# Kernel tuning notes

Measured on AMD Instinct MI355X. Metric: run time of the kernel, lower is better.

Reference implementation:

```python
import jax, jax.numpy as jnp
import numpy as np
import math

# dims: batch, in-channels, freq bins, frames(=cropsize), ffn dim, bands
B, C, BINS, W, FF, NB = 16, 8, 1024, 256, 2048, 4
EPS = 1e-5


def _ln(x, g, b):
    m = x.mean(-1, keepdims=True)
    v = ((x - m) ** 2).mean(-1, keepdims=True)
    return (x - m) / jnp.sqrt(v + EPS) * g + b


def _conv1d(x, w, groups=1):
    # x: [b, Cin, L], w: [Cout, Cin//groups, K], 'same' padding
    pad = (w.shape[-1] - 1) // 2
    return jax.lax.conv_general_dilated(
        x, w, (1,), [(pad, pad)],
        dimension_numbers=('NCH', 'OIH', 'NCH'), feature_group_count=groups)


def _mb_attn(x, mem, qw, qb, kw, kb, vw, vb, ow, ob, er, dist_w):
    # MultibandFrameAttention with skewed relative-position bias
    b, w, c = x.shape
    d = c // NB
    q = (x @ qw.T + qb).reshape(b, w, NB, d).transpose(0, 2, 1, 3)    # [b,nb,w,d]
    k = (mem @ kw.T + kb).reshape(b, w, NB, d).transpose(0, 2, 3, 1)  # [b,nb,d,w]
    v = (mem @ vw.T + vb).reshape(b, w, NB, d).transpose(0, 2, 1, 3)  # [b,nb,w,d]
    # skew trick: q @ er -> pad left on last dim -> transpose -> drop first row
    qer = jnp.einsum('bnwd,dc->bnwc', q, er)                           # [b,nb,w,W]
    skew = jnp.pad(qer, ((0, 0), (0, 0), (0, 0), (1, 0)))
    skew = skew.transpose(0, 1, 3, 2)[:, :, 1:, :]                     # [b,nb,W,w]
    idx = jnp.arange(w)
    dist = jnp.abs(idx[:, None] - idx[None, :]).astype(x.dtype) / 2.0  # [w,w]
    p = dist[None] * dist_w + skew                                     # [b,nb,w,w]
    qk = jnp.einsum('bnwd,bndk->bnwk', q, k) / math.sqrt(c)
    a = jax.nn.softmax(qk + p, axis=-1)
    o = jnp.einsum('bnwk,bnkd->bnwd', a, v).transpose(0, 2, 1, 3).reshape(b, w, c)
    return o @ ow.T + ob


def setup_inputs() -> dict:
    key = jax.random.key(0)
    ks = jax.random.split(key, 24)
    rn = lambda k, s, sc=0.02: jax.random.normal(k, s, dtype=jnp.float32) * sc
    d = BINS // NB
    ones = lambda n: jnp.ones((n,), jnp.float32)
    zeros = lambda n: jnp.zeros((n,), jnp.float32)
    return {
        'x': jax.random.normal(ks[0], (B, C, BINS, W), jnp.float32),
        'bott_w': rn(ks[1], (1, C), 0.3),
        'bn_g': ones(1), 'bn_b': zeros(1), 'bn_m': zeros(1), 'bn_v': ones(1),
        'glu_w': rn(ks[2], (2 * BINS, BINS)),
        'n1g': ones(BINS), 'n1b': zeros(BINS),
        'c1L_w': rn(ks[3], (2 * FF, BINS)),
        'c1R_w': rn(ks[4], (FF // 2, BINS, 3)),
        'n2g': ones(2 * FF), 'n2b': zeros(2 * FF),
        'c2dw_w': rn(ks[5], (2 * FF, 1, 9), 0.1),
        'c2pw_w': rn(ks[6], (FF // 2, 2 * FF)),
        'n3g': ones(BINS), 'n3b': zeros(BINS),
        'qw': rn(ks[7], (BINS, BINS)), 'qb': zeros(BINS),
        'kw': rn(ks[8], (BINS, BINS)), 'kb': zeros(BINS),
        'vw': rn(ks[9], (BINS, BINS)), 'vb': zeros(BINS),
        'ow': rn(ks[10], (BINS, BINS)), 'ob': zeros(BINS),
        'er': rn(ks[11], (d, W), 0.02),
        'dist_w': rn(ks[12], (NB, W, 1), 0.02),
        'n4g': ones(BINS), 'n4b': zeros(BINS),
        'c3_w': rn(ks[13], (2 * FF, BINS)),
        'c4_w': rn(ks[14], (BINS, 2 * FF)),
        'n5g': ones(BINS), 'n5b': zeros(BINS),
    }


def reference(x, bott_w, bn_g, bn_b, bn_m, bn_v, glu_w, n1g, n1b,
              c1L_w, c1R_w, n2g, n2b, c2dw_w, c2pw_w, n3g, n3b,
              qw, qb, kw, kb, vw, vb, ow, ob, er, dist_w,
              n4g, n4b, c3_w, c4_w, n5g, n5b):
    # bottleneck: Linear(C->1) over channel dim, BatchNorm2d(1) eval, ReLU
    h0 = jnp.einsum('bchw,oc->bohw', x, bott_w)                        # [b,1,bins,w]
    h0 = (h0 - bn_m[None, :, None, None]) / jnp.sqrt(bn_v[None, :, None, None] + EPS)
    h0 = jax.nn.relu(h0 * bn_g[None, :, None, None] + bn_b[None, :, None, None])
    xs = h0[:, 0].transpose(0, 2, 1)                                   # [b,w,bins]

    # GLU block
    g = xs @ glu_w.T
    a, bgate = g[..., :BINS], g[..., BINS:]
    xs = _ln(xs + a * jax.nn.sigmoid(bgate), n1g, n1b)

    # conv/linear FFN
    hL = jax.nn.relu(xs @ c1L_w.T)                                     # [b,w,2ff]
    hR = jax.nn.relu(_conv1d(xs.transpose(0, 2, 1), c1R_w).transpose(0, 2, 1))
    hR = jnp.pad(hR, ((0, 0), (0, 0), (0, hL.shape[2] - hR.shape[2])))
    h = _ln(hL + hR, n2g, n2b)
    t = _conv1d(h.transpose(0, 2, 1), c2dw_w, groups=2 * FF)           # depthwise
    t = jnp.einsum('bcl,oc->bol', t, c2pw_w).transpose(0, 2, 1)        # [b,w,ff//2]
    t = jnp.pad(t, ((0, 0), (0, 0), (0, xs.shape[2] - t.shape[2])))
    xs = _ln(xs + t, n3g, n3b)

    # multiband attention (self)
    h = _mb_attn(xs, xs, qw, qb, kw, kb, vw, vb, ow, ob, er, dist_w)
    xs = _ln(xs + h, n4g, n4b)

    # final FFN
    h = jax.nn.relu(xs @ c3_w.T) @ c4_w.T
    xs = _ln(xs + h, n5g, n5b)
    return xs.transpose(0, 2, 1)[:, None]                              # [b,1,bins,w]
```

## Files before the change

### kernel.cpp

```cpp
#include <hip/hip_runtime.h>
#include <hip/hip_bf16.h>

#define EPSF 1e-5f

typedef unsigned short u16;
typedef unsigned int   u32;
typedef __attribute__((ext_vector_type(8))) short bf16x8;
typedef __attribute__((ext_vector_type(4))) float f32x4;

#define SWZ(row) (((row) & 7) << 3)

__device__ __forceinline__ u16 f2bf(float f) {
    u32 u = __builtin_bit_cast(u32, f);
    u32 r = u + 0x7fffu + ((u >> 16) & 1u);
    return (u16)(r >> 16);
}
__device__ __forceinline__ float bf2f(u16 h) {
    return __builtin_bit_cast(float, (u32)h << 16);
}
__device__ __forceinline__ float4 bf4f(ushort4 v) {
    return make_float4(bf2f(v.x), bf2f(v.y), bf2f(v.z), bf2f(v.w));
}
__device__ __forceinline__ ushort4 f4bf(float a, float b, float c, float d) {
    ushort4 o; o.x = f2bf(a); o.y = f2bf(b); o.z = f2bf(c); o.w = f2bf(d); return o;
}
__device__ __forceinline__ void gld16(void* lds, const void* gsrc) {
    __builtin_amdgcn_global_load_lds(
        (const __attribute__((address_space(1))) u32*)gsrc,
        (__attribute__((address_space(3))) u32*)lds, 16, 0, 0);
}

__device__ __forceinline__ float wred_sum(float v) {
#pragma unroll
    for (int off = 32; off; off >>= 1) v += __shfl_xor(v, off, 64);
    return v;
}
__device__ __forceinline__ void block_red2(float& s1, float& s2, int tid) {
    __shared__ float red[8];
    s1 = wred_sum(s1); s2 = wred_sum(s2);
    const int lane = tid & 63, wid = tid >> 6;
    if (!lane) { red[wid] = s1; red[4 + wid] = s2; }
    __syncthreads();
    s1 = red[0] + red[1] + red[2] + red[3];
    s2 = red[4] + red[5] + red[6] + red[7];
}

struct SetupArgs {
    const float* ws[9]; u16* wd[9]; int wn[9];
    const float* c1r; u16* c1rd;
    const float* er;  u16* erd;
    const float* dw;  float* dwd;
    const float* qb;  const float* kb; const float* vb; float* bcat;
    u16* zp;
    int off[15];
};
__global__ __launch_bounds__(256)
void setup_k(SetupArgs a)
{
    const int b = blockIdx.x;
    int seg = 0;
    while (seg < 13 && b >= a.off[seg + 1]) ++seg;
    const int i = (b - a.off[seg]) * 256 + threadIdx.x;
    if (seg < 9) {
        if (i < a.wn[seg]) {
            const float4 v = ((const float4*)a.ws[seg])[i];
            const float s = (seg == 6) ? 0.03125f : 1.f;
            ((ushort4*)a.wd[seg])[i] = f4bf(v.x * s, v.y * s, v.z * s, v.w * s);
        }
    } else if (seg == 9) {
        if (i < 3145728) {
            const int q = i / 3072, rem = i - q * 3072;
            const int ks = rem >> 10, ci = rem & 1023;
            a.c1rd[i] = f2bf(a.c1r[((long)q * 1024 + ci) * 3 + ks]);
        }
    } else if (seg == 10) {
        if (i < 65536) { const int c = i >> 8, d = i & 255; a.erd[i] = f2bf(a.er[d * 256 + c]); }
    } else if (seg == 11) {
        if (i < 36864) { const int k = i >> 12, c = i & 4095; a.dwd[i] = a.dw[c * 9 + k]; }
    } else if (seg == 12) {
        if (i < 3072) {
            const float* s = (i < 1024) ? a.qb : ((i < 2048) ? a.kb : a.vb);
            float v = s[i & 1023];
            if (i >= 1024 && i < 2048) v *= 0.03125f;
            a.bcat[i] = v;
        }
    } else {
        if (i < 8192) a.zp[i] = 0;
    }
}

__global__ __launch_bounds__(256)
void bottleneck_k(const float* __restrict__ x, const float* __restrict__ bw,
                  const float* __restrict__ bn_g, const float* __restrict__ bn_b,
                  const float* __restrict__ bn_m, const float* __restrict__ bn_v,
                  u16* __restrict__ xsb)
{
    __shared__ float tile[32][33];
    const int b = blockIdx.z, h0 = blockIdx.y * 32, w0 = blockIdx.x * 32;
    const int tid = threadIdx.x, c = tid & 31, r = tid >> 5;
    float wreg[8];
#pragma unroll
    for (int ch = 0; ch < 8; ++ch) wreg[ch] = bw[ch];
    const float sc = bn_g[0] * rsqrtf(bn_v[0] + EPSF);
    const float sh = bn_b[0] - bn_m[0] * sc;
#pragma unroll
    for (int it = 0; it < 4; ++it) {
        const int h = h0 + r + it * 8;
        const int w = w0 + c;
        float acc = 0.f;
#pragma unroll
        for (int ch = 0; ch < 8; ++ch)
            acc += x[(((long)b * 8 + ch) * 1024 + h) * 256 + w] * wreg[ch];
        tile[r + it * 8][c] = fmaxf(acc * sc + sh, 0.f);
    }
    __syncthreads();
#pragma unroll
    for (int it = 0; it < 4; ++it) {
        const int wl = r + it * 8;
        xsb[((long)b * 256 + w0 + wl) * 1024 + h0 + c] = f2bf(tile[c][wl]);
    }
}

template<int ACT, int OUTBF, int BIAS, int SPLITK>
__global__ __launch_bounds__(512, 2)
void gemm8_k(const u16* __restrict__ A, const u16* __restrict__ B,
             const float* __restrict__ bias, void* __restrict__ Cout,
             int N, int K , int lda, int ldb, long partStride)
{
    extern __shared__ u16 lds[];
    const int m0 = blockIdx.y * 256, n0 = blockIdx.x * 256;
    const int koff = (SPLITK > 1) ? blockIdx.z * K : 0;
    const int nt = K >> 6;
    const int tid = threadIdx.x;
    const int lane = tid & 63, wid = tid >> 6;
    const int wr = ((wid >> 2) & 1) * 128;
    const int wc = (wid & 3) * 64;
    const int l15 = lane & 15, l4 = lane >> 4;

    const u16* Ag = A + (long)m0 * lda + koff;
    const u16* Bg = B + (long)n0 * ldb + koff;

    auto stage = [&](const u16* g, int ld, int ldsbase, int kcol, int h) {
#pragma unroll
        for (int is = 0; is < 2; ++is) {
            const int r = h * 128 + is * 64 + (tid >> 3);
            const int sc = ((tid & 7) * 8) ^ SWZ(r);
            gld16(&lds[ldsbase + h * 8192 + is * 4096 + tid * 8],
                  g + (long)r * ld + kcol + sc);
        }
    };
    auto frag = [&](int base, int row, int col) -> bf16x8 {
        return *(const bf16x8*)&lds[base + row * 64 + (col ^ SWZ(row))];
    };

    f32x4 acc[8][4] = {};

    stage(Ag, lda, 0, 0, 0);
    stage(Ag, lda, 0, 0, 1);
    stage(Bg, ldb, 32768, 0, 0);
    stage(Bg, ldb, 32768, 0, 1);
    if (nt > 1) {
        stage(Bg, ldb, 49152, 64, 0);
        stage(Bg, ldb, 49152, 64, 1);
        stage(Ag, lda, 16384, 64, 0);
        asm volatile("s_waitcnt vmcnt(6)" ::: "memory");
    } else {
        asm volatile("s_waitcnt vmcnt(0)" ::: "memory");
    }
    __builtin_amdgcn_s_barrier();

    for (int kt = 0; kt < nt; ++kt) {
        const int cs = kt & 1;
        const int ab = cs * 16384;
        const int bb = 32768 + cs * 16384;
        const int abn = (cs ^ 1) * 16384;
        const int kc1 = (kt + 1) * 64, kc2 = (kt + 2) * 64;
        bf16x8 alo[4][2], ahi[4][2], b01[2][2], b23[2][2];

#pragma unroll
        for (int i = 0; i < 4; ++i)
#pragma unroll
            for (int kk = 0; kk < 2; ++kk)
                alo[i][kk] = frag(ab, wr + i * 16 + l15, kk * 32 + l4 * 8);
#pragma unroll
        for (int j = 0; j < 2; ++j)
#pragma unroll
            for (int kk = 0; kk < 2; ++kk)
                b01[j][kk] = frag(bb, wc + j * 16 + l15, kk * 32 + l4 * 8);
        if (kt + 1 < nt) stage(Ag, lda, abn, kc1, 1);
        __builtin_amdgcn_s_barrier();
        asm volatile("s_waitcnt lgkmcnt(0)" ::: "memory");
        __builtin_amdgcn_s_setprio(1);
#pragma unroll
        for (int i = 0; i < 4; ++i)
#pragma unroll
            for (int j = 0; j < 2; ++j)
#pragma unroll
                for (int kk = 0; kk < 2; ++kk)
                    acc[i][j] = __builtin_amdgcn_mfma_f32_16x16x32_bf16(alo[i][kk], b01[j][kk], acc[i][j], 0, 0, 0);
        __builtin_amdgcn_s_setprio(0);
        __builtin_amdgcn_s_barrier();

#pragma unroll
        for (int j = 0; j < 2; ++j)
#pragma unroll
            for (int kk = 0; kk < 2; ++kk)
                b23[j][kk] = frag(bb, wc + (j + 2) * 16 + l15, kk * 32 + l4 * 8);
        if (kt + 2 < nt) stage(Bg, ldb, bb, kc2, 0);
        __builtin_amdgcn_s_barrier();
        asm volatile("s_waitcnt lgkmcnt(0)" ::: "memory");
        __builtin_amdgcn_s_setprio(1);
#pragma unroll
        for (int i = 0; i < 4; ++i)
#pragma unroll
            for (int j = 0; j < 2; ++j)
#pragma unroll
                for (int kk = 0; kk < 2; ++kk)
                    acc[i][j + 2] = __builtin_amdgcn_mfma_f32_16x16x32_bf16(alo[i][kk], b23[j][kk], acc[i][j + 2], 0, 0, 0);
        __builtin_amdgcn_s_setprio(0);
        __builtin_amdgcn_s_barrier();

#pragma unroll
        for (int i = 0; i < 4; ++i)
#pragma unroll
            for (int kk = 0; kk < 2; ++kk)
                ahi[i][kk] = frag(ab, wr + (i + 4) * 16 + l15, kk * 32 + l4 * 8);
        if (kt + 2 < nt) stage(Bg, ldb, bb, kc2, 1);
        __builtin_amdgcn_s_barrier();
        asm volatile("s_waitcnt lgkmcnt(0)" ::: "memory");
        __builtin_amdgcn_s_setprio(1);
#pragma unroll
        for (int i = 0; i < 4; ++i)
#pragma unroll
            for (int j = 0; j < 2; ++j)
#pragma unroll
                for (int kk = 0; kk < 2; ++kk)
                    acc[i + 4][j + 2] = __builtin_amdgcn_mfma_f32_16x16x32_bf16(ahi[i][kk], b23[j][kk], acc[i + 4][j + 2], 0, 0, 0);
        __builtin_amdgcn_s_setprio(0);
        __builtin_amdgcn_s_barrier();

        if (kt + 2 < nt) stage(Ag, lda, ab, kc2, 0);
        __builtin_amdgcn_s_barrier();
        __builtin_amdgcn_s_setprio(1);
#pragma unroll
        for (int i = 0; i < 4; ++i)
#pragma unroll
            for (int j = 0; j < 2; ++j)
#pragma unroll
                for (int kk = 0; kk < 2; ++kk)
                    acc[i + 4][j] = __builtin_amdgcn_mfma_f32_16x16x32_bf16(ahi[i][kk], b01[j][kk], acc[i + 4][j], 0, 0, 0);
        __builtin_amdgcn_s_setprio(0);
        if (kt + 2 < nt) {
            asm volatile("s_waitcnt vmcnt(6)" ::: "memory");
        } else {
            asm volatile("s_waitcnt vmcnt(0)" ::: "memory");
        }
        __builtin_amdgcn_s_barrier();
    }

    if (SPLITK > 1) {
        u16* Cp = (u16*)Cout + (long)blockIdx.z * partStride;
#pragma unroll
        for (int i = 0; i < 8; ++i)
#pragma unroll
            for (int j = 0; j < 4; ++j) {
                const int n = n0 + wc + j * 16 + l15;
#pragma unroll
                for (int q = 0; q < 4; ++q) {
                    const int m = m0 + wr + i * 16 + l4 * 4 + q;
                    Cp[(long)m * N + n] = f2bf(acc[i][j][q]);
                }
            }
    } else {
        float* Cf = (float*)Cout;
        u16*   Cb = (u16*)Cout;
#pragma unroll
        for (int i = 0; i < 8; ++i)
#pragma unroll
            for (int j = 0; j < 4; ++j) {
                const int n = n0 + wc + j * 16 + l15;
                const float bv = BIAS ? bias[n] : 0.f;
#pragma unroll
                for (int q = 0; q < 4; ++q) {
                    const int m = m0 + wr + i * 16 + l4 * 4 + q;
                    float v = acc[i][j][q] + bv;
                    if (ACT) v = fmaxf(v, 0.f);
                    if (OUTBF) Cb[(long)m * N + n] = f2bf(v);
                    else       Cf[(long)m * N + n] = v;
                }
            }
    }
}

__global__ __launch_bounds__(512, 2)
void ffconv8_k(const u16* __restrict__ Xb, const u16* __restrict__ Wl,
               const u16* __restrict__ Wr, const u16* __restrict__ zp,
               u16* __restrict__ Hout, u16* __restrict__ Cp3)
{
    extern __shared__ u16 lds[];
    const int bx = blockIdx.x;
    const int m0 = blockIdx.y * 256;
    const bool conv = bx >= 16;
    const int tap  = conv ? ((bx - 16) >> 2) : 0;
    const int shift = conv ? (tap - 1) : 0;
    const int n0 = conv ? (((bx - 16) & 3) * 256) : (bx * 256);
    const u16* Bbase = conv ? (Wr + (long)n0 * 3072 + tap * 1024)
                            : (Wl + (long)n0 * 1024);
    const int ldb = conv ? 3072 : 1024;
    const int nt = 16;
    const int tid = threadIdx.x;
    const int lane = tid & 63, wid = tid >> 6;
    const int wr = ((wid >> 2) & 1) * 128;
    const int wc = (wid & 3) * 64;
    const int l15 = lane & 15, l4 = lane >> 4;

    auto stageA = [&](int ldsbase, int kcol, int h) {
#pragma unroll
        for (int is = 0; is < 2; ++is) {
            const int r = h * 128 + is * 64 + (tid >> 3);
            const int sc = ((tid & 7) * 8) ^ SWZ(r);
            const int t = m0 + r;
            const int wp = (t & 255) + shift;
            const u16* src = ((unsigned)wp < 256u)
                ? Xb + (long)(t + shift) * 1024 + kcol + sc
                : zp;
            gld16(&lds[ldsbase + h * 8192 + is * 4096 + tid * 8], src);
        }
    };
    auto stageB = [&](int ldsbase, int kcol, int h) {
#pragma unroll
        for (int is = 0; is < 2; ++is) {
            const int r = h * 128 + is * 64 + (tid >> 3);
            const int sc = ((tid & 7) * 8) ^ SWZ(r);
            gld16(&lds[ldsbase + h * 8192 + is * 4096 + tid * 8],
                  Bbase + (long)r * ldb + kcol + sc);
        }
    };
    auto frag = [&](int base, int row, int col) -> bf16x8 {
        return *(const bf16x8*)&lds[base + row * 64 + (col ^ SWZ(row))];
    };

    f32x4 acc[8][4] = {};

    stageA(0, 0, 0);
    stageA(0, 0, 1);
    stageB(32768, 0, 0);
    stageB(32768, 0, 1);
    stageB(49152, 64, 0);
    stageB(49152, 64, 1);
    stageA(16384, 64, 0);
    asm volatile("s_waitcnt vmcnt(6)" ::: "memory");
    __builtin_amdgcn_s_barrier();

    for (int kt = 0; kt < nt; ++kt) {
        const int cs = kt & 1;
        const int ab = cs * 16384;
        const int bb = 32768 + cs * 16384;
        const int abn = (cs ^ 1) * 16384;
        const int kc1 = (kt + 1) * 64, kc2 = (kt + 2) * 64;
        bf16x8 alo[4][2], ahi[4][2], b01[2][2], b23[2][2];

#pragma unroll
        for (int i = 0; i < 4; ++i)
#pragma unroll
            for (int kk = 0; kk < 2; ++kk)
                alo[i][kk] = frag(ab, wr + i * 16 + l15, kk * 32 + l4 * 8);
#pragma unroll
        for (int j = 0; j < 2; ++j)
#pragma unroll
            for (int kk = 0; kk < 2; ++kk)
                b01[j][kk] = frag(bb, wc + j * 16 + l15, kk * 32 + l4 * 8);
        if (kt + 1 < nt) stageA(abn, kc1, 1);
        __builtin_amdgcn_s_barrier();
        asm volatile("s_waitcnt lgkmcnt(0)" ::: "memory");
        __builtin_amdgcn_s_setprio(1);
#pragma unroll
        for (int i = 0; i < 4; ++i)
#pragma unroll
            for (int j = 0; j < 2; ++j)
#pragma unroll
                for (int kk = 0; kk < 2; ++kk)
                    acc[i][j] = __builtin_amdgcn_mfma_f32_16x16x32_bf16(alo[i][kk], b01[j][kk], acc[i][j], 0, 0, 0);
        __builtin_amdgcn_s_setprio(0);
        __builtin_amdgcn_s_barrier();

#pragma unroll
        for (int j = 0; j < 2; ++j)
#pragma unroll
            for (int kk = 0; kk < 2; ++kk)
                b23[j][kk] = frag(bb, wc + (j + 2) * 16 + l15, kk * 32 + l4 * 8);
        if (kt + 2 < nt) stageB(bb, kc2, 0);
        __builtin_amdgcn_s_barrier();
        asm volatile("s_waitcnt lgkmcnt(0)" ::: "memory");
        __builtin_amdgcn_s_setprio(1);
#pragma unroll
        for (int i = 0; i < 4; ++i)
#pragma unroll
            for (int j = 0; j < 2; ++j)
#pragma unroll
                for (int kk = 0; kk < 2; ++kk)
                    acc[i][j + 2] = __builtin_amdgcn_mfma_f32_16x16x32_bf16(alo[i][kk], b23[j][kk], acc[i][j + 2], 0, 0, 0);
        __builtin_amdgcn_s_setprio(0);
        __builtin_amdgcn_s_barrier();

#pragma unroll
        for (int i = 0; i < 4; ++i)
#pragma unroll
            for (int kk = 0; kk < 2; ++kk)
                ahi[i][kk] = frag(ab, wr + (i + 4) * 16 + l15, kk * 32 + l4 * 8);
        if (kt + 2 < nt) stageB(bb, kc2, 1);
        __builtin_amdgcn_s_barrier();
        asm volatile("s_waitcnt lgkmcnt(0)" ::: "memory");
        __builtin_amdgcn_s_setprio(1);
#pragma unroll
        for (int i = 0; i < 4; ++i)
#pragma unroll
            for (int j = 0; j < 2; ++j)
#pragma unroll
                for (int kk = 0; kk < 2; ++kk)
                    acc[i + 4][j + 2] = __builtin_amdgcn_mfma_f32_16x16x32_bf16(ahi[i][kk], b23[j][kk], acc[i + 4][j + 2], 0, 0, 0);
        __builtin_amdgcn_s_setprio(0);
        __builtin_amdgcn_s_barrier();

        if (kt + 2 < nt) stageA(ab, kc2, 0);
        __builtin_amdgcn_s_barrier();
        __builtin_amdgcn_s_setprio(1);
#pragma unroll
        for (int i = 0; i < 4; ++i)
#pragma unroll
            for (int j = 0; j < 2; ++j)
#pragma unroll
                for (int kk = 0; kk < 2; ++kk)
                    acc[i + 4][j] = __builtin_amdgcn_mfma_f32_16x16x32_bf16(ahi[i][kk], b01[j][kk], acc[i + 4][j], 0, 0, 0);
        __builtin_amdgcn_s_setprio(0);
        if (kt + 2 < nt) {
            asm volatile("s_waitcnt vmcnt(6)" ::: "memory");
        } else {
            asm volatile("s_waitcnt vmcnt(0)" ::: "memory");
        }
        __builtin_amdgcn_s_barrier();
    }

    if (conv) {
        u16* Cp = Cp3 + (long)tap * 4194304;
#pragma unroll
        for (int i = 0; i < 8; ++i)
#pragma unroll
            for (int j = 0; j < 4; ++j) {
                const int n = n0 + wc + j * 16 + l15;
#pragma unroll
                for (int q = 0; q < 4; ++q) {
                    const int m = m0 + wr + i * 16 + l4 * 4 + q;
                    Cp[(long)m * 1024 + n] = f2bf(acc[i][j][q]);
                }
            }
    } else {
#pragma unroll
        for (int i = 0; i < 8; ++i)
#pragma unroll
            for (int j = 0; j < 4; ++j) {
                const int n = n0 + wc + j * 16 + l15;
#pragma unroll
                for (int q = 0; q < 4; ++q) {
                    const int m = m0 + wr + i * 16 + l4 * 4 + q;
                    Hout[(long)m * 4096 + n] = f2bf(fmaxf(acc[i][j][q], 0.f));
                }
            }
    }
}

__global__ __launch_bounds__(256, 2)
void attn_fused_k(const u16* __restrict__ QKVb, const u16* __restrict__ erT,
                  const u16* __restrict__ Vt, const float* __restrict__ dwp,
                  u16* __restrict__ Oc)
{
    __shared__ __align__(16) u16 As[4096];
    __shared__ __align__(16) u16 Bs[16384];
    __shared__ __align__(16) u16 Pl[16384];
    __shared__ float redM[4][64];
    __shared__ float redS[4][64];
    const int z = blockIdx.y, zb = z >> 2, zn = z & 3;
    const int m0 = blockIdx.x * 64;
    const int tid = threadIdx.x;
    const int lane = tid & 63, wid = tid >> 6;
    const int l15 = lane & 15, l4 = lane >> 4;

    const u16* Qg = QKVb + (long)(zb * 256) * 3072 + zn * 256;
    const u16* Kg = Qg + 1024;

    auto stageA64 = [&](const u16* g, long ld) {
#pragma unroll
        for (int p = 0; p < 2; ++p) {
            const int e = p * 2048 + tid * 8;
            const int r = e >> 6, c = e & 63;
            const int sc = c ^ SWZ(r);
            gld16(&As[e], g + (long)r * ld + sc);
        }
    };
    auto stageB256 = [&](const u16* g, long ld) {
#pragma unroll
        for (int p = 0; p < 8; ++p) {
            const int e = p * 2048 + tid * 8;
            const int r = e >> 6, c = e & 63;
            const int sc = c ^ SWZ(r);
            gld16(&Bs[e], g + (long)r * ld + sc);
        }
    };
    auto fragA = [&](int i, int kk) -> bf16x8 {
        const int row = i * 16 + l15, col = kk * 32 + l4 * 8;
        return *(const bf16x8*)&As[row * 64 + (col ^ SWZ(row))];
    };
    auto fragB = [&](int j, int kk) -> bf16x8 {
        const int row = wid * 64 + j * 16 + l15, col = kk * 32 + l4 * 8;
        return *(const bf16x8*)&Bs[row * 64 + (col ^ SWZ(row))];
    };
    auto fragP = [&](int kc, int i, int kk) -> bf16x8 {
        const int row = i * 16 + l15, col = kk * 32 + l4 * 8;
        return *(const bf16x8*)&Pl[kc * 4096 + row * 64 + (col ^ SWZ(row))];
    };

    f32x4 acc1[4][4] = {};

    for (int kc = 0; kc < 8; ++kc) {
        __syncthreads();
        if (kc < 4) {
            stageA64(Qg + (long)m0 * 3072 + kc * 64, 3072);
            stageB256(Kg + kc * 64, 3072);
        } else {
            stageA64(erT + (long)m0 * 256 + (kc - 4) * 64, 256);
            stageB256(Qg + (kc - 4) * 64, 3072);
        }
        __syncthreads();
#pragma unroll
        for (int i = 0; i < 4; ++i) {
            const bf16x8 a0 = fragA(i, 0), a1 = fragA(i, 1);
#pragma unroll
            for (int j = 0; j < 4; ++j) {
                acc1[i][j] = __builtin_amdgcn_mfma_f32_16x16x32_bf16(a0, fragB(j, 0), acc1[i][j], 0, 0, 0);
                acc1[i][j] = __builtin_amdgcn_mfma_f32_16x16x32_bf16(a1, fragB(j, 1), acc1[i][j], 0, 0, 0);
            }
        }
    }

#pragma unroll
    for (int i = 0; i < 4; ++i)
#pragma unroll
        for (int q = 0; q < 4; ++q) {
            const int mg = m0 + i * 16 + l4 * 4 + q;
            const float dw = dwp[zn * 256 + mg];
#pragma unroll
            for (int j = 0; j < 4; ++j) {
                const int ng = wid * 64 + j * 16 + l15;
                acc1[i][j][q] += fabsf((float)(mg - ng)) * 0.5f * dw;
            }
        }

    float rmax[4][4], rsum[4][4];
#pragma unroll
    for (int i = 0; i < 4; ++i)
#pragma unroll
        for (int q = 0; q < 4; ++q) {
            float mv = fmaxf(fmaxf(acc1[i][0][q], acc1[i][1][q]),
                             fmaxf(acc1[i][2][q], acc1[i][3][q]));
#pragma unroll
            for (int off = 1; off <= 8; off <<= 1) mv = fmaxf(mv, __shfl_xor(mv, off, 64));
            rmax[i][q] = mv;
        }
    if (l15 == 0) {
#pragma unroll
        for (int i = 0; i < 4; ++i)
#pragma unroll
            for (int q = 0; q < 4; ++q)
                redM[wid][i * 16 + l4 * 4 + q] = rmax[i][q];
    }
    __syncthreads();
#pragma unroll
    for (int i = 0; i < 4; ++i)
#pragma unroll
        for (int q = 0; q < 4; ++q) {
            const int ml = i * 16 + l4 * 4 + q;
            rmax[i][q] = fmaxf(fmaxf(redM[0][ml], redM[1][ml]), fmaxf(redM[2][ml], redM[3][ml]));
        }
#pragma unroll
    for (int i = 0; i < 4; ++i)
#pragma unroll
        for (int q = 0; q < 4; ++q) {
            float sv = 0.f;
#pragma unroll
            for (int j = 0; j < 4; ++j) {
                const float e = __expf(acc1[i][j][q] - rmax[i][q]);
                acc1[i][j][q] = e;
                sv += e;
            }
#pragma unroll
            for (int off = 1; off <= 8; off <<= 1) sv += __shfl_xor(sv, off, 64);
            rsum[i][q] = sv;
        }
    if (l15 == 0) {
#pragma unroll
        for (int i = 0; i < 4; ++i)
#pragma unroll
            for (int q = 0; q < 4; ++q)
                redS[wid][i * 16 + l4 * 4 + q] = rsum[i][q];
    }
    __syncthreads();
#pragma unroll
    for (int i = 0; i < 4; ++i)
#pragma unroll
        for (int q = 0; q < 4; ++q) {
            const int ml = i * 16 + l4 * 4 + q;
            rsum[i][q] = redS[0][ml] + redS[1][ml] + redS[2][ml] + redS[3][ml];
        }
#pragma unroll
    for (int i = 0; i < 4; ++i)
#pragma unroll
        for (int q = 0; q < 4; ++q) {
            const float rinv = 1.f / rsum[i][q];
            const int ml = i * 16 + l4 * 4 + q;
#pragma unroll
            for (int j = 0; j < 4; ++j) {
                const int nc = j * 16 + l15;
                Pl[wid * 4096 + ml * 64 + (nc ^ SWZ(ml))] = f2bf(acc1[i][j][q] * rinv);
            }
        }
    __syncthreads();

    f32x4 accO[4][4] = {};
    for (int kc = 0; kc < 4; ++kc) {
        __syncthreads();
        stageB256(Vt + (long)(z * 256) * 256 + kc * 64, 256);
        __syncthreads();
#pragma unroll
        for (int i = 0; i < 4; ++i) {
            const bf16x8 a0 = fragP(kc, i, 0), a1 = fragP(kc, i, 1);
#pragma unroll
            for (int j = 0; j < 4; ++j) {
                accO[i][j] = __builtin_amdgcn_mfma_f32_16x16x32_bf16(a0, fragB(j, 0), accO[i][j], 0, 0, 0);
                accO[i][j] = __builtin_amdgcn_mfma_f32_16x16x32_bf16(a1, fragB(j, 1), accO[i][j], 0, 0, 0);
            }
        }
    }

#pragma unroll
    for (int i = 0; i < 4; ++i)
#pragma unroll
        for (int j = 0; j < 4; ++j) {
            const int d = wid * 64 + j * 16 + l15;
#pragma unroll
            for (int q = 0; q < 4; ++q) {
                const int mg = m0 + i * 16 + l4 * 4 + q;
                Oc[(long)(zb * 256 + mg) * 1024 + zn * 256 + d] = f2bf(accO[i][j][q]);
            }
        }
}

__global__ __launch_bounds__(256)
void glu_ln_k(const u16* __restrict__ xs0, const u16* __restrict__ g2,
              const float* __restrict__ gam, const float* __restrict__ bet,
              u16* __restrict__ outb)
{
    const int t = blockIdx.x, tid = threadIdx.x;
    const int f0 = tid * 4;
    const long PS = 8388608;
    const float4 xv = bf4f(*(const ushort4*)&xs0[(long)t * 1024 + f0]);
    const float4 a0 = bf4f(*(const ushort4*)&g2[(long)t * 2048 + f0]);
    const float4 g0 = bf4f(*(const ushort4*)&g2[(long)t * 2048 + 1024 + f0]);
    const float4 a1 = bf4f(*(const ushort4*)&g2[PS + (long)t * 2048 + f0]);
    const float4 g1 = bf4f(*(const ushort4*)&g2[PS + (long)t * 2048 + 1024 + f0]);
    const float ax = a0.x + a1.x, ay = a0.y + a1.y, az = a0.z + a1.z, aw = a0.w + a1.w;
    const float gx = g0.x + g1.x, gy = g0.y + g1.y, gz = g0.z + g1.z, gw = g0.w + g1.w;
    float vals[4];
    vals[0] = xv.x + ax / (1.f + expf(-gx));
    vals[1] = xv.y + ay / (1.f + expf(-gy));
    vals[2] = xv.z + az / (1.f + expf(-gz));
    vals[3] = xv.w + aw / (1.f + expf(-gw));
    float s1 = vals[0] + vals[1] + vals[2] + vals[3];
    float s2 = vals[0]*vals[0] + vals[1]*vals[1] + vals[2]*vals[2] + vals[3]*vals[3];
    block_red2(s1, s2, tid);
    const float mean = s1 * (1.f / 1024.f);
    const float var  = s2 * (1.f / 1024.f) - mean * mean;
    const float rstd = rsqrtf(var + EPSF);
    const float4 gm = *(const float4*)&gam[f0];
    const float4 bt = *(const float4*)&bet[f0];
    *(ushort4*)&outb[(long)t * 1024 + f0] = f4bf(
        (vals[0] - mean) * rstd * gm.x + bt.x,
        (vals[1] - mean) * rstd * gm.y + bt.y,
        (vals[2] - mean) * rstd * gm.z + bt.z,
        (vals[3] - mean) * rstd * gm.w + bt.w);
}

template<int P, int BIAS>
__global__ __launch_bounds__(256)
void add_ln1024_k(const u16* __restrict__ A, const u16* __restrict__ Bp,
                  const float* __restrict__ bias,
                  const float* __restrict__ gam, const float* __restrict__ bet,
                  u16* __restrict__ outb)
{
    const int t = blockIdx.x, tid = threadIdx.x;
    const int f0 = tid * 4;
    const long PS = 4194304;
    const float4 a = bf4f(*(const ushort4*)&A[(long)t * 1024 + f0]);
    float4 b = bf4f(*(const ushort4*)&Bp[(long)t * 1024 + f0]);
#pragma unroll
    for (int p = 1; p < P; ++p) {
        const float4 bp = bf4f(*(const ushort4*)&Bp[p * PS + (long)t * 1024 + f0]);
        b.x += bp.x; b.y += bp.y; b.z += bp.z; b.w += bp.w;
    }
    if (BIAS) {
        const float4 bb = *(const float4*)&bias[f0];
        b.x += bb.x; b.y += bb.y; b.z += bb.z; b.w += bb.w;
    }
    float vals[4] = {a.x + b.x, a.y + b.y, a.z + b.z, a.w + b.w};
    float s1 = vals[0] + vals[1] + vals[2] + vals[3];
    float s2 = vals[0]*vals[0] + vals[1]*vals[1] + vals[2]*vals[2] + vals[3]*vals[3];
    block_red2(s1, s2, tid);
    const float mean = s1 * (1.f / 1024.f);
    const float var  = s2 * (1.f / 1024.f) - mean * mean;
    const float rstd = rsqrtf(var + EPSF);
    const float4 gm = *(const float4*)&gam[f0];
    const float4 bt = *(const float4*)&bet[f0];
    *(ushort4*)&outb[(long)t * 1024 + f0] = f4bf(
        (vals[0] - mean) * rstd * gm.x + bt.x,
        (vals[1] - mean) * rstd * gm.y + bt.y,
        (vals[2] - mean) * rstd * gm.z + bt.z,
        (vals[3] - mean) * rstd * gm.w + bt.w);
}

__global__ __launch_bounds__(256)
void add_ln4096_k(const u16* __restrict__ A, const u16* __restrict__ Bp,
                  const float* __restrict__ gam, const float* __restrict__ bet,
                  u16* __restrict__ outb)
{
    const int t = blockIdx.x, tid = threadIdx.x;
    const long PS = 4194304;
    const int f0 = tid * 16;
    float vals[16];
    const bf16x8 a0 = *(const bf16x8*)&A[(long)t * 4096 + f0];
    const bf16x8 a1 = *(const bf16x8*)&A[(long)t * 4096 + f0 + 8];
#pragma unroll
    for (int e = 0; e < 8; ++e) { vals[e] = bf2f((u16)a0[e]); vals[8 + e] = bf2f((u16)a1[e]); }
    if (tid < 64) {
#pragma unroll
        for (int c = 0; c < 4; ++c) {
            const int fc = f0 + c * 4;
            const float4 b0 = bf4f(*(const ushort4*)&Bp[(long)t * 1024 + fc]);
            const float4 b1 = bf4f(*(const ushort4*)&Bp[PS + (long)t * 1024 + fc]);
            const float4 b2 = bf4f(*(const ushort4*)&Bp[2 * PS + (long)t * 1024 + fc]);
            vals[c*4+0] += fmaxf(b0.x + b1.x + b2.x, 0.f);
            vals[c*4+1] += fmaxf(b0.y + b1.y + b2.y, 0.f);
            vals[c*4+2] += fmaxf(b0.z + b1.z + b2.z, 0.f);
            vals[c*4+3] += fmaxf(b0.w + b1.w + b2.w, 0.f);
        }
    }
    float s1 = 0.f, s2 = 0.f;
#pragma unroll
    for (int e = 0; e < 16; ++e) { s1 += vals[e]; s2 += vals[e] * vals[e]; }
    block_red2(s1, s2, tid);
    const float mean = s1 * (1.f / 4096.f);
    const float var  = s2 * (1.f / 4096.f) - mean * mean;
    const float rstd = rsqrtf(var + EPSF);
#pragma unroll
    for (int c = 0; c < 4; ++c) {
        const int fc = f0 + c * 4;
        const float4 gm = *(const float4*)&gam[fc];
        const float4 bt = *(const float4*)&bet[fc];
        *(ushort4*)&outb[(long)t * 4096 + fc] = f4bf(
            (vals[c*4+0] - mean) * rstd * gm.x + bt.x,
            (vals[c*4+1] - mean) * rstd * gm.y + bt.y,
            (vals[c*4+2] - mean) * rstd * gm.z + bt.z,
            (vals[c*4+3] - mean) * rstd * gm.w + bt.w);
    }
}

__global__ __launch_bounds__(256)
void dwconv8_k(const u16* __restrict__ h, const float* __restrict__ wT,
               u16* __restrict__ out)
{
    const long idx = (long)blockIdx.x * 256 + threadIdx.x;
    const int cg = (int)(idx & 511);
    const int t  = (int)(idx >> 9);
    const int w  = t & 255;
    const int c0 = cg * 8;
    float acc[8] = {};
#pragma unroll
    for (int k = 0; k < 9; ++k) {
        const int wp = w + k - 4;
        if ((unsigned)wp < 256u) {
            const bf16x8 hv = *(const bf16x8*)&h[(long)(t + k - 4) * 4096 + c0];
            const float4 w0 = *(const float4*)&wT[k * 4096 + c0];
            const float4 w1 = *(const float4*)&wT[k * 4096 + c0 + 4];
            acc[0] += bf2f((u16)hv[0]) * w0.x;
            acc[1] += bf2f((u16)hv[1]) * w0.y;
            acc[2] += bf2f((u16)hv[2]) * w0.z;
            acc[3] += bf2f((u16)hv[3]) * w0.w;
            acc[4] += bf2f((u16)hv[4]) * w1.x;
            acc[5] += bf2f((u16)hv[5]) * w1.y;
            acc[6] += bf2f((u16)hv[6]) * w1.z;
            acc[7] += bf2f((u16)hv[7]) * w1.w;
        }
    }
    bf16x8 res;
#pragma unroll
    for (int j = 0; j < 8; ++j) res[j] = (short)f2bf(acc[j]);
    *(bf16x8*)&out[(long)t * 4096 + c0] = res;
}

__global__ __launch_bounds__(256)
void vtrans_k(const u16* __restrict__ QKVb, u16* __restrict__ Vt)
{
    __shared__ u16 t[32][33];
    const int z = blockIdx.z, zb = z >> 2, zn = z & 3;
    const int w0 = blockIdx.x * 32, d0 = blockIdx.y * 32;
    const int tid = threadIdx.x, c = tid & 31, r = tid >> 5;
#pragma unroll
    for (int it = 0; it < 4; ++it) {
        const int wl = r + it * 8;
        t[wl][c] = QKVb[(long)(zb * 256 + w0 + wl) * 3072 + 2048 + zn * 256 + d0 + c];
    }
    __syncthreads();
#pragma unroll
    for (int it = 0; it < 4; ++it) {
        const int dl = r + it * 8;
        Vt[((long)z * 256 + d0 + dl) * 256 + w0 + c] = t[c][dl];
    }
}

__global__ __launch_bounds__(256)
void transpose_out_k(const u16* __restrict__ xs, float* __restrict__ out)
{
    __shared__ u16 tile[32][34];
    const int b = blockIdx.z, f0 = blockIdx.y * 32, w0 = blockIdx.x * 32;
    const int tid = threadIdx.x, c = tid & 31, r = tid >> 5;
#pragma unroll
    for (int it = 0; it < 4; ++it) {
        const int w = w0 + r + it * 8;
        tile[r + it * 8][c] = xs[((long)b * 256 + w) * 1024 + f0 + c];
    }
    __syncthreads();
#pragma unroll
    for (int it = 0; it < 4; ++it) {
        const int fl = r + it * 8;
        out[((long)b * 1024 + f0 + fl) * 256 + w0 + c] = bf2f(tile[c][fl]);
    }
}

extern "C" void kernel_launch(void* const* d_in, const int* in_sizes, int n_in,
                              void* d_out, int out_size, void* d_ws, size_t ws_size,
                              hipStream_t stream)
{
    const float* x      = (const float*)d_in[0];
    const float* bott_w = (const float*)d_in[1];
    const float* bn_g   = (const float*)d_in[2];
    const float* bn_b   = (const float*)d_in[3];
    const float* bn_m   = (const float*)d_in[4];
    const float* bn_v   = (const float*)d_in[5];
    const float* glu_w  = (const float*)d_in[6];
    const float* n1g    = (const float*)d_in[7];
    const float* n1b    = (const float*)d_in[8];
    const float* c1L_w  = (const float*)d_in[9];
    const float* c1R_w  = (const float*)d_in[10];
    const float* n2g    = (const float*)d_in[11];
    const float* n2b    = (const float*)d_in[12];
    const float* c2dw_w = (const float*)d_in[13];
    const float* c2pw_w = (const float*)d_in[14];
    const float* n3g    = (const float*)d_in[15];
    const float* n3b    = (const float*)d_in[16];
    const float* qw     = (const float*)d_in[17];
    const float* qb     = (const float*)d_in[18];
    const float* kw     = (const float*)d_in[19];
    const float* kb     = (const float*)d_in[20];
    const float* vw     = (const float*)d_in[21];
    const float* vb     = (const float*)d_in[22];
    const float* ow     = (const float*)d_in[23];
    const float* ob     = (const float*)d_in[24];
    const float* er     = (const float*)d_in[25];
    const float* dist_w = (const float*)d_in[26];
    const float* n4g    = (const float*)d_in[27];
    const float* n4b    = (const float*)d_in[28];
    const float* c3_w   = (const float*)d_in[29];
    const float* c4_w   = (const float*)d_in[30];
    const float* n5g    = (const float*)d_in[31];
    const float* n5b    = (const float*)d_in[32];
    float* out = (float*)d_out;

    char* Wb_ = (char*)d_ws;
    auto Bf = [&](size_t mib) { return (u16*)(Wb_ + (mib << 20)); };
    u16* XA   = Bf(0);
    u16* XB   = Bf(8);
    u16* H0b  = Bf(32);
    u16* Hglu = Bf(64);
    u16* C3p  = Bf(64);
    u16* P4   = Bf(64);
    u16* H1b  = Bf(128);
    u16* Hdw  = Bf(160);
    u16* QKVb = Bf(192);
    u16* Vt   = Bf(216);
    u16* S1b  = Bf(264);
    u16* wGLU = Bf(296); u16* wC1L = Bf(300); u16* wC1R = Bf(308);
    u16* wC2P = Bf(314); u16* wQKV = Bf(322); u16* wO   = Bf(328);
    u16* wC3  = Bf(330); u16* wC4  = Bf(338);
    u16* erT  = Bf(346);
    u16* zp   = (u16*)(Wb_ + (346u << 20) + 131072);
    float* wdwT = (float*)(Wb_ + (346u << 20) + 131072 + 16384);
    float* bQKV = (float*)(Wb_ + (346u << 20) + 131072 + 16384 + 147456);

    const dim3 blk(256);
    const dim3 blk8(512);
    const long PS1 = 4194304;
    const size_t SH8 = 131072;

    SetupArgs sa;
    sa.ws[0] = glu_w;  sa.wd[0] = wGLU;            sa.wn[0] = 524288;
    sa.ws[1] = c1L_w;  sa.wd[1] = wC1L;            sa.wn[1] = 1048576;
    sa.ws[2] = c2pw_w; sa.wd[2] = wC2P;            sa.wn[2] = 1048576;
    sa.ws[3] = c3_w;   sa.wd[3] = wC3;             sa.wn[3] = 1048576;
    sa.ws[4] = c4_w;   sa.wd[4] = wC4;             sa.wn[4] = 1048576;
    sa.ws[5] = qw;     sa.wd[5] = wQKV;            sa.wn[5] = 262144;
    sa.ws[6] = kw;     sa.wd[6] = wQKV + 1048576;  sa.wn[6] = 262144;
    sa.ws[7] = vw;     sa.wd[7] = wQKV + 2097152;  sa.wn[7] = 262144;
    sa.ws[8] = ow;     sa.wd[8] = wO;              sa.wn[8] = 262144;
    sa.c1r = c1R_w; sa.c1rd = wC1R;
    sa.er  = er;    sa.erd  = erT;
    sa.dw  = c2dw_w; sa.dwd = wdwT;
    sa.qb = qb; sa.kb = kb; sa.vb = vb; sa.bcat = bQKV;
    sa.zp = zp;
    {
        int bc[14] = {2048, 4096, 4096, 4096, 4096, 1024, 1024, 1024, 1024,
                      12288, 256, 144, 12, 32};
        int acc = 0;
        for (int s = 0; s < 14; ++s) { sa.off[s] = acc; acc += bc[s]; }
        sa.off[14] = acc;
        setup_k<<<dim3(acc), blk, 0, stream>>>(sa);
    }

    bottleneck_k<<<dim3(8, 32, 16), blk, 0, stream>>>(x, bott_w, bn_g, bn_b, bn_m, bn_v, XA);

    gemm8_k<0,0,0,2><<<dim3(8, 16, 2), blk8, SH8, stream>>>(XA, wGLU, nullptr, Hglu,
        2048, 512, 1024, 1024, (long)4096 * 2048);

    glu_ln_k<<<dim3(4096), blk, 0, stream>>>(XA, Hglu, n1g, n1b, XB);

    ffconv8_k<<<dim3(28, 16), blk8, SH8, stream>>>(XB, wC1L, wC1R, zp, H0b, C3p);

    add_ln4096_k<<<dim3(4096), blk, 0, stream>>>(H0b, C3p, n2g, n2b, H1b);

    dwconv8_k<<<dim3(8192), blk, 0, stream>>>(H1b, wdwT, Hdw);

    gemm8_k<0,0,0,4><<<dim3(4, 16, 4), blk8, SH8, stream>>>(Hdw, wC2P, nullptr, P4,
        1024, 1024, 4096, 4096, PS1);

    add_ln1024_k<4,0><<<dim3(4096), blk, 0, stream>>>(XB, P4, nullptr, n3g, n3b, XA);

    gemm8_k<0,1,1,1><<<dim3(12, 16, 1), blk8, SH8, stream>>>(XA, wQKV, bQKV, QKVb,
        3072, 1024, 1024, 1024, 0);

    vtrans_k<<<dim3(8, 8, 64), blk, 0, stream>>>(QKVb, Vt);

    attn_fused_k<<<dim3(4, 64), blk, 0, stream>>>(QKVb, erT, Vt, dist_w, S1b);

    gemm8_k<0,0,0,4><<<dim3(4, 16, 4), blk8, SH8, stream>>>(S1b, wO, nullptr, P4,
        1024, 256, 1024, 1024, PS1);

    add_ln1024_k<4,1><<<dim3(4096), blk, 0, stream>>>(XA, P4, ob, n4g, n4b, XB);

    gemm8_k<1,1,0,1><<<dim3(16, 16, 1), blk8, SH8, stream>>>(XB, wC3, nullptr, H0b,
        4096, 1024, 1024, 1024, 0);

    gemm8_k<0,0,0,4><<<dim3(4, 16, 4), blk8, SH8, stream>>>(H0b, wC4, nullptr, P4,
        1024, 1024, 4096, 4096, PS1);

    add_ln1024_k<4,0><<<dim3(4096), blk, 0, stream>>>(XB, P4, nullptr, n5g, n5b, XA);

    transpose_out_k<<<dim3(8, 32, 16), blk, 0, stream>>>(XA, out);

    (void)in_sizes; (void)n_in; (void)out_size; (void)ws_size;
}
```

Before: 468.3 us.

## Fuse V transpose into QKV GEMM epilogue and vectorize bottleneck loads

The QKV projection GEMM gains a templated epilogue. For output tiles in the V column range it adds the bias and writes transposed bf16 data straight into the Vt buffer, so the separate vtrans_k kernel launch and its read/write of the V slice go away. The bottleneck 1x1 conv kernel now has each thread load a float4 of four consecutive frames per channel instead of scalar loads, which cuts the number of global load instructions. The transposed epilogue writes 8-byte chunks with a strided pattern, so store coalescing may be worse than the old dedicated transpose kernel.

```diff
diff --git a/kernel.cpp b/kernel.cpp
--- a/kernel.cpp
+++ b/kernel.cpp
@@ -97,23 +97,26 @@
 {
     __shared__ float tile[32][33];
     const int b = blockIdx.z, h0 = blockIdx.y * 32, w0 = blockIdx.x * 32;
-    const int tid = threadIdx.x, c = tid & 31, r = tid >> 5;
+    const int tid = threadIdx.x;
+    const int tw = tid & 7, th = tid >> 3;
     float wreg[8];
 #pragma unroll
     for (int ch = 0; ch < 8; ++ch) wreg[ch] = bw[ch];
     const float sc = bn_g[0] * rsqrtf(bn_v[0] + EPSF);
     const float sh = bn_b[0] - bn_m[0] * sc;
-#pragma unroll
-    for (int it = 0; it < 4; ++it) {
-        const int h = h0 + r + it * 8;
-        const int w = w0 + c;
-        float acc = 0.f;
-#pragma unroll
-        for (int ch = 0; ch < 8; ++ch)
-            acc += x[(((long)b * 8 + ch) * 1024 + h) * 256 + w] * wreg[ch];
-        tile[r + it * 8][c] = fmaxf(acc * sc + sh, 0.f);
-    }
+    float4 acc = make_float4(0.f, 0.f, 0.f, 0.f);
+#pragma unroll
+    for (int ch = 0; ch < 8; ++ch) {
+        const float4 v = *(const float4*)&x[(((long)b * 8 + ch) * 1024 + h0 + th) * 256 + w0 + tw * 4];
+        acc.x += v.x * wreg[ch]; acc.y += v.y * wreg[ch];
+        acc.z += v.z * wreg[ch]; acc.w += v.w * wreg[ch];
+    }
+    tile[th][tw * 4 + 0] = fmaxf(acc.x * sc + sh, 0.f);
+    tile[th][tw * 4 + 1] = fmaxf(acc.y * sc + sh, 0.f);
+    tile[th][tw * 4 + 2] = fmaxf(acc.z * sc + sh, 0.f);
+    tile[th][tw * 4 + 3] = fmaxf(acc.w * sc + sh, 0.f);
     __syncthreads();
+    const int c = tid & 31, r = tid >> 5;
 #pragma unroll
     for (int it = 0; it < 4; ++it) {
         const int wl = r + it * 8;
@@ -121,11 +124,12 @@
     }
 }
 
-template<int ACT, int OUTBF, int BIAS, int SPLITK>
+template<int ACT, int OUTBF, int BIAS, int SPLITK, int VOUT>
 __global__ __launch_bounds__(512, 2)
 void gemm8_k(const u16* __restrict__ A, const u16* __restrict__ B,
              const float* __restrict__ bias, void* __restrict__ Cout,
-             int N, int K , int lda, int ldb, long partStride)
+             int N, int K , int lda, int ldb, long partStride,
+             u16* __restrict__ Vtp)
 {
     extern __shared__ u16 lds[];
     const int m0 = blockIdx.y * 256, n0 = blockIdx.x * 256;
@@ -258,7 +262,21 @@
         __builtin_amdgcn_s_barrier();
     }
 
-    if (SPLITK > 1) {
+    if (VOUT && n0 >= 2048) {
+        const int zb4 = (m0 >> 8) * 4;
+#pragma unroll
+        for (int i = 0; i < 8; ++i)
+#pragma unroll
+            for (int j = 0; j < 4; ++j) {
+                const int n = n0 + wc + j * 16 + l15;
+                const int d = n - 2048, zn = d >> 8, dl = d & 255;
+                const float bv = BIAS ? bias[n] : 0.f;
+                const int w = wr + i * 16 + l4 * 4;
+                ushort4 st = f4bf(acc[i][j][0] + bv, acc[i][j][1] + bv,
+                                  acc[i][j][2] + bv, acc[i][j][3] + bv);
+                *(ushort4*)&Vtp[((long)(zb4 + zn) * 256 + dl) * 256 + w] = st;
+            }
+    } else if (SPLITK > 1) {
         u16* Cp = (u16*)Cout + (long)blockIdx.z * partStride;
 #pragma unroll
         for (int i = 0; i < 8; ++i)
@@ -803,26 +821,6 @@
 #pragma unroll
     for (int j = 0; j < 8; ++j) res[j] = (short)f2bf(acc[j]);
     *(bf16x8*)&out[(long)t * 4096 + c0] = res;
-}
-
-__global__ __launch_bounds__(256)
-void vtrans_k(const u16* __restrict__ QKVb, u16* __restrict__ Vt)
-{
-    __shared__ u16 t[32][33];
-    const int z = blockIdx.z, zb = z >> 2, zn = z & 3;
-    const int w0 = blockIdx.x * 32, d0 = blockIdx.y * 32;
-    const int tid = threadIdx.x, c = tid & 31, r = tid >> 5;
-#pragma unroll
-    for (int it = 0; it < 4; ++it) {
-        const int wl = r + it * 8;
-        t[wl][c] = QKVb[(long)(zb * 256 + w0 + wl) * 3072 + 2048 + zn * 256 + d0 + c];
-    }
-    __syncthreads();
-#pragma unroll
-    for (int it = 0; it < 4; ++it) {
-        const int dl = r + it * 8;
-        Vt[((long)z * 256 + d0 + dl) * 256 + w0 + c] = t[c][dl];
-    }
 }
 
 __global__ __launch_bounds__(256)
@@ -935,8 +933,8 @@
 
     bottleneck_k<<<dim3(8, 32, 16), blk, 0, stream>>>(x, bott_w, bn_g, bn_b, bn_m, bn_v, XA);
 
-    gemm8_k<0,0,0,2><<<dim3(8, 16, 2), blk8, SH8, stream>>>(XA, wGLU, nullptr, Hglu,
-        2048, 512, 1024, 1024, (long)4096 * 2048);
+    gemm8_k<0,0,0,2,0><<<dim3(8, 16, 2), blk8, SH8, stream>>>(XA, wGLU, nullptr, Hglu,
+        2048, 512, 1024, 1024, (long)4096 * 2048, nullptr);
 
     glu_ln_k<<<dim3(4096), blk, 0, stream>>>(XA, Hglu, n1g, n1b, XB);
 
@@ -946,28 +944,26 @@
 
     dwconv8_k<<<dim3(8192), blk, 0, stream>>>(H1b, wdwT, Hdw);
 
-    gemm8_k<0,0,0,4><<<dim3(4, 16, 4), blk8, SH8, stream>>>(Hdw, wC2P, nullptr, P4,
-        1024, 1024, 4096, 4096, PS1);
+    gemm8_k<0,0,0,4,0><<<dim3(4, 16, 4), blk8, SH8, stream>>>(Hdw, wC2P, nullptr, P4,
+        1024, 1024, 4096, 4096, PS1, nullptr);
 
     add_ln1024_k<4,0><<<dim3(4096), blk, 0, stream>>>(XB, P4, nullptr, n3g, n3b, XA);
 
-    gemm8_k<0,1,1,1><<<dim3(12, 16, 1), blk8, SH8, stream>>>(XA, wQKV, bQKV, QKVb,
-        3072, 1024, 1024, 1024, 0);
-
-    vtrans_k<<<dim3(8, 8, 64), blk, 0, stream>>>(QKVb, Vt);
+    gemm8_k<0,1,1,1,1><<<dim3(12, 16, 1), blk8, SH8, stream>>>(XA, wQKV, bQKV, QKVb,
+        3072, 1024, 1024, 1024, 0, Vt);
 
     attn_fused_k<<<dim3(4, 64), blk, 0, stream>>>(QKVb, erT, Vt, dist_w, S1b);
 
-    gemm8_k<0,0,0,4><<<dim3(4, 16, 4), blk8, SH8, stream>>>(S1b, wO, nullptr, P4,
-        1024, 256, 1024, 1024, PS1);
+    gemm8_k<0,0,0,4,0><<<dim3(4, 16, 4), blk8, SH8, stream>>>(S1b, wO, nullptr, P4,
+        1024, 256, 1024, 1024, PS1, nullptr);
 
     add_ln1024_k<4,1><<<dim3(4096), blk, 0, stream>>>(XA, P4, ob, n4g, n4b, XB);
 
-    gemm8_k<1,1,0,1><<<dim3(16, 16, 1), blk8, SH8, stream>>>(XB, wC3, nullptr, H0b,
-        4096, 1024, 1024, 1024, 0);
-
-    gemm8_k<0,0,0,4><<<dim3(4, 16, 4), blk8, SH8, stream>>>(H0b, wC4, nullptr, P4,
-        1024, 1024, 4096, 4096, PS1);
+    gemm8_k<1,1,0,1,0><<<dim3(16, 16, 1), blk8, SH8, stream>>>(XB, wC3, nullptr, H0b,
+        4096, 1024, 1024, 1024, 0, nullptr);
+
+    gemm8_k<0,0,0,4,0><<<dim3(4, 16, 4), blk8, SH8, stream>>>(H0b, wC4, nullptr, P4,
+        1024, 1024, 4096, 4096, PS1, nullptr);
 
     add_ln1024_k<4,0><<<dim3(4096), blk, 0, stream>>>(XB, P4, nullptr, n5g, n5b, XA);
 
```

Result: no change. 464.6 us (median of 2 runs) (-0.8%).
